# Kernel tuning notes

Measured on AMD Instinct MI355X. Metric: run time of the kernel, lower is better.

The kernel has to match this reference:

```python
import jax, jax.numpy as jnp
import numpy as np

N_NODES = 50000
N_EDGES = 800000
IN_DIM = 128
HID = 128
LATENT = 64
N_LAYERS = 3
N_GRAPHS = 256
BN_EPS = 1e-5


def setup_inputs() -> dict:
    key = jax.random.key(0)
    ks = jax.random.split(key, 12)
    x = jax.random.normal(ks[0], (N_NODES, IN_DIM), dtype=jnp.float32)
    edge_index = jax.random.randint(ks[1], (2, N_EDGES), 0, N_NODES, dtype=jnp.int32)
    batch = jnp.sort(jax.random.randint(ks[2], (N_NODES,), 0, N_GRAPHS, dtype=jnp.int32))
    s = 1.0 / np.sqrt(HID)
    # stacked per-layer SAGEConv params: lin_l (neighbor path, with bias), lin_r (root path)
    Wl = jax.random.uniform(ks[3], (N_LAYERS, HID, HID), jnp.float32, -s, s)
    bl = jax.random.uniform(ks[4], (N_LAYERS, HID), jnp.float32, -s, s)
    Wr = jax.random.uniform(ks[5], (N_LAYERS, HID, HID), jnp.float32, -s, s)
    gamma = jnp.ones((HID,), jnp.float32)
    beta = jnp.zeros((HID,), jnp.float32)
    fcW = jax.random.uniform(ks[6], (HID, LATENT), jnp.float32, -s, s)
    fcb = jax.random.uniform(ks[7], (LATENT,), jnp.float32, -s, s)
    return {"x": x, "edge_index": edge_index, "batch": batch, "Wl": Wl, "bl": bl,
            "Wr": Wr, "gamma": gamma, "beta": beta, "fcW": fcW, "fcb": fcb}


def _sage_conv(x, src, dst, Wl_i, bl_i, Wr_i):
    # mean-aggregate source features into target nodes (PyG SAGEConv, aggr='mean')
    agg = jax.ops.segment_sum(x[src], dst, num_segments=N_NODES)  # [N, D]
    cnt = jax.ops.segment_sum(jnp.ones((src.shape[0],), x.dtype), dst, num_segments=N_NODES)
    mean = agg / jnp.maximum(cnt, 1.0)[:, None]
    return mean @ Wl_i + bl_i + x @ Wr_i


def reference(x, edge_index, batch, Wl, bl, Wr, gamma, beta, fcW, fcb):
    src, dst = edge_index[0], edge_index[1]
    h = x
    for i in range(N_LAYERS):
        h = _sage_conv(h, src, dst, Wl[i], bl[i], Wr[i])
        h = jax.nn.relu(h)  # dropout: identity at inference
    # global_add_pool over graphs
    pooled = jax.ops.segment_sum(h, batch, num_segments=N_GRAPHS)  # [G, HID]
    # BatchNorm1d over the graph dimension (batch statistics)
    mu = pooled.mean(axis=0)
    var = pooled.var(axis=0)
    normed = (pooled - mu) * jax.lax.rsqrt(var + BN_EPS) * gamma + beta
    return normed @ fcW + fcb
```

## Files before the change

kernel.cpp:

```cpp
#include <hip/hip_runtime.h>
#include <cstdint>
#include <cstddef>

constexpr int HID = 128;
constexpr int LATENT = 64;
constexpr int BSHIFT = 7;
constexpr int NBUCK_MAX = 512;
constexpr int EPB = 1024;

typedef __attribute__((ext_vector_type(8))) short short8;
typedef __attribute__((ext_vector_type(4))) float f32x4;

__device__ inline unsigned short f2bf(float f) {
    unsigned u = __float_as_uint(f);
    u += 0x7fff + ((u >> 16) & 1);
    return (unsigned short)(u >> 16);
}
__device__ inline unsigned pack_bf16x2(float lo, float hi) {
    unsigned ulo = __float_as_uint(lo);
    unsigned uhi = __float_as_uint(hi);
    ulo += 0x7fff + ((ulo >> 16) & 1);
    uhi += 0x7fff + ((uhi >> 16) & 1);
    return (ulo >> 16) | (uhi & 0xffff0000u);
}

__global__ __launch_bounds__(256) void stage1_k(const int* __restrict__ dst,
                                                const float* __restrict__ x,
                                                const float* __restrict__ Wl,
                                                const float* __restrict__ Wr,
                                                int* __restrict__ partial,
                                                unsigned* __restrict__ hx2,
                                                unsigned short* __restrict__ WT,
                                                int nE, int nbuck, int ebB, int n2x) {
    if (blockIdx.x < (unsigned)ebB) {
        __shared__ int lh[NBUCK_MAX];
        for (int b = threadIdx.x; b < nbuck; b += 256) lh[b] = 0;
        __syncthreads();
        int base = blockIdx.x * EPB;
        int end = min(base + EPB, nE);
        for (int i = base + threadIdx.x; i < end; i += 256)
            atomicAdd(&lh[dst[i] >> BSHIFT], 1);
        __syncthreads();
        int* row = partial + (size_t)blockIdx.x * NBUCK_MAX;
        for (int b = threadIdx.x; b < nbuck; b += 256) row[b] = lh[b];
    } else if (blockIdx.x < (unsigned)(ebB + 384)) {
        int idx = (blockIdx.x - ebB) * 256 + threadIdx.x;
        int l = idx / (128 * 256);
        int rem = idx % (128 * 256);
        int n = rem / 256;
        int k = rem % 256;
        float v = (k < 128) ? Wl[(size_t)l * 128 * 128 + (size_t)k * 128 + n]
                            : Wr[(size_t)l * 128 * 128 + (size_t)(k - 128) * 128 + n];
        WT[idx] = f2bf(v);
    } else {
        int i = (blockIdx.x - ebB - 384) * 256 + threadIdx.x;
        if (i < n2x) {
            float2 v = ((const float2*)x)[i];
            hx2[i] = pack_bf16x2(v.x, v.y);
        }
    }
}

__global__ __launch_bounds__(256) void colscan_k(int* __restrict__ partial,
                                                 int* __restrict__ bucketTotal, int ebB) {
    int b = blockIdx.x;
    int t = threadIdx.x;
    const int CH = (ebB + 255) / 256;
    int vals[8];
    int s = 0;
    #pragma unroll
    for (int c = 0; c < 8; ++c) {
        if (c >= CH) break;
        int k = t * CH + c;
        int v = (k < ebB) ? partial[(size_t)k * NBUCK_MAX + b] : 0;
        vals[c] = v; s += v;
    }
    __shared__ int part[256];
    part[t] = s;
    __syncthreads();
    for (int d = 1; d < 256; d <<= 1) {
        int u = (t >= d) ? part[t - d] : 0;
        __syncthreads();
        if (t >= d) part[t] += u;
        __syncthreads();
    }
    int run = (t == 0) ? 0 : part[t - 1];
    #pragma unroll
    for (int c = 0; c < 8; ++c) {
        if (c >= CH) break;
        int k = t * CH + c;
        if (k < ebB) partial[(size_t)k * NBUCK_MAX + b] = run;
        run += vals[c];
    }
    if (t == 255) bucketTotal[b] = run;
}

__global__ __launch_bounds__(512) void bscan2_k(const int* __restrict__ bucketTotal,
                                                int* __restrict__ bucketStart,
                                                int* __restrict__ row_ptr,
                                                int nbuck, int nE, int nN) {
    __shared__ int part[512];
    int t = threadIdx.x;
    int v = (t < nbuck) ? bucketTotal[t] : 0;
    part[t] = v;
    __syncthreads();
    for (int d = 1; d < 512; d <<= 1) {
        int u = (t >= d) ? part[t - d] : 0;
        __syncthreads();
        if (t >= d) part[t] += u;
        __syncthreads();
    }
    if (t < nbuck) bucketStart[t] = part[t] - v;
    if (t == 0) { bucketStart[nbuck] = nE; row_ptr[nN] = nE; }
}

__global__ __launch_bounds__(256) void bplace_k(const int* __restrict__ src,
                                                const int* __restrict__ dst,
                                                const int* __restrict__ partial,
                                                const int* __restrict__ bucketStart,
                                                uint2* __restrict__ staged, int nE, int nbuck) {
    __shared__ int lh[NBUCK_MAX];
    __shared__ int lb[NBUCK_MAX];
    for (int b = threadIdx.x; b < nbuck; b += 256) lh[b] = 0;
    __syncthreads();
    int base = blockIdx.x * EPB;
    int end = min(base + EPB, nE);
    const int* myPre = partial + (size_t)blockIdx.x * NBUCK_MAX;
    for (int b = threadIdx.x; b < nbuck; b += 256)
        lb[b] = bucketStart[b] + myPre[b];
    __syncthreads();
    for (int i = base + threadIdx.x; i < end; i += 256) {
        int d = dst[i];
        int b = d >> BSHIFT;
        int loc = atomicAdd(&lh[b], 1);
        staged[lb[b] + loc] = make_uint2((unsigned)src[i], (unsigned)d);
    }
}

__global__ __launch_bounds__(256) void sort_bucket_k(const uint2* __restrict__ staged,
                                                     const int* __restrict__ bucketStart,
                                                     int* __restrict__ row_ptr,
                                                     float* __restrict__ inv,
                                                     int* __restrict__ csr_src, int nN) {
    __shared__ int cnt[128];
    __shared__ int rp[128];
    int g = blockIdx.x;
    int beg = bucketStart[g], end = bucketStart[g + 1];
    if (threadIdx.x < 128) cnt[threadIdx.x] = 0;
    __syncthreads();
    for (int i = beg + threadIdx.x; i < end; i += 256)
        atomicAdd(&cnt[staged[i].y & 127], 1);
    __syncthreads();
    if (threadIdx.x < 128) rp[threadIdx.x] = cnt[threadIdx.x];
    __syncthreads();
    #pragma unroll
    for (int d = 1; d < 128; d <<= 1) {
        int v = 0;
        if (threadIdx.x < 128 && threadIdx.x >= d) v = rp[threadIdx.x - d];
        __syncthreads();
        if (threadIdx.x < 128 && threadIdx.x >= d) rp[threadIdx.x] += v;
        __syncthreads();
    }
    if (threadIdx.x < 128) {
        int c = cnt[threadIdx.x];
        int excl = rp[threadIdx.x] - c;
        int node = (g << BSHIFT) + threadIdx.x;
        if (node < nN) {
            row_ptr[node] = beg + excl;
            inv[node] = 1.0f / fmaxf((float)c, 1.0f);
        }
        cnt[threadIdx.x] = excl;
    }
    __syncthreads();
    for (int i = beg + threadIdx.x; i < end; i += 256) {
        uint2 e = staged[i];
        int pos = atomicAdd(&cnt[e.y & 127], 1);
        csr_src[beg + pos] = (int)e.x;
    }
}

__global__ __launch_bounds__(256) void gather_k(const int* __restrict__ row_ptr,
                                                const int* __restrict__ csr_src,
                                                const float* __restrict__ inv,
                                                const uint4* __restrict__ h4,
                                                uint4* __restrict__ mean4, int nN) {
    int w = blockIdx.x * 4 + (threadIdx.x >> 6);
    if (w >= nN) return;
    int lane = threadIdx.x & 63;
    int quarter = lane >> 4;
    int col = lane & 15;
    int beg = row_ptr[w], end = row_ptr[w + 1];
    float accA[8] = {}, accB[8] = {}, accC[8] = {}, accD[8] = {};
    for (int base = beg; base < end; base += 64) {
        int navail = min(64, end - base);
        int idx = (lane < navail) ? csr_src[base + lane] : 0;
        for (int j = 0; j < navail; j += 16) {
            int e0 = j + quarter;
            int e1 = j + 4 + quarter;
            int e2 = j + 8 + quarter;
            int e3 = j + 12 + quarter;
            int s0 = __shfl(idx, min(e0, navail - 1), 64);
            int s1 = __shfl(idx, min(e1, navail - 1), 64);
            int s2 = __shfl(idx, min(e2, navail - 1), 64);
            int s3 = __shfl(idx, min(e3, navail - 1), 64);
            uint4 u0 = h4[(size_t)s0 * 16 + col];
            uint4 u1 = h4[(size_t)s1 * 16 + col];
            uint4 u2 = h4[(size_t)s2 * 16 + col];
            uint4 u3 = h4[(size_t)s3 * 16 + col];
            if (e0 < navail) {
                accA[0] += __uint_as_float(u0.x << 16); accA[1] += __uint_as_float(u0.x & 0xffff0000u);
                accA[2] += __uint_as_float(u0.y << 16); accA[3] += __uint_as_float(u0.y & 0xffff0000u);
                accA[4] += __uint_as_float(u0.z << 16); accA[5] += __uint_as_float(u0.z & 0xffff0000u);
                accA[6] += __uint_as_float(u0.w << 16); accA[7] += __uint_as_float(u0.w & 0xffff0000u);
            }
            if (e1 < navail) {
                accB[0] += __uint_as_float(u1.x << 16); accB[1] += __uint_as_float(u1.x & 0xffff0000u);
                accB[2] += __uint_as_float(u1.y << 16); accB[3] += __uint_as_float(u1.y & 0xffff0000u);
                accB[4] += __uint_as_float(u1.z << 16); accB[5] += __uint_as_float(u1.z & 0xffff0000u);
                accB[6] += __uint_as_float(u1.w << 16); accB[7] += __uint_as_float(u1.w & 0xffff0000u);
            }
            if (e2 < navail) {
                accC[0] += __uint_as_float(u2.x << 16); accC[1] += __uint_as_float(u2.x & 0xffff0000u);
                accC[2] += __uint_as_float(u2.y << 16); accC[3] += __uint_as_float(u2.y & 0xffff0000u);
                accC[4] += __uint_as_float(u2.z << 16); accC[5] += __uint_as_float(u2.z & 0xffff0000u);
                accC[6] += __uint_as_float(u2.w << 16); accC[7] += __uint_as_float(u2.w & 0xffff0000u);
            }
            if (e3 < navail) {
                accD[0] += __uint_as_float(u3.x << 16); accD[1] += __uint_as_float(u3.x & 0xffff0000u);
                accD[2] += __uint_as_float(u3.y << 16); accD[3] += __uint_as_float(u3.y & 0xffff0000u);
                accD[4] += __uint_as_float(u3.z << 16); accD[5] += __uint_as_float(u3.z & 0xffff0000u);
                accD[6] += __uint_as_float(u3.w << 16); accD[7] += __uint_as_float(u3.w & 0xffff0000u);
            }
        }
    }
    #pragma unroll
    for (int k = 0; k < 8; ++k) {
        float v = (accA[k] + accB[k]) + (accC[k] + accD[k]);
        v += __shfl_xor(v, 16, 64);
        v += __shfl_xor(v, 32, 64);
        accA[k] = v;
    }
    if (quarter == 0) {
        float iv = inv[w];
        uint4 o;
        o.x = pack_bf16x2(accA[0] * iv, accA[1] * iv);
        o.y = pack_bf16x2(accA[2] * iv, accA[3] * iv);
        o.z = pack_bf16x2(accA[4] * iv, accA[5] * iv);
        o.w = pack_bf16x2(accA[6] * iv, accA[7] * iv);
        mean4[(size_t)w * 16 + col] = o;
    }
}

__global__ __launch_bounds__(256) void sage_mfma_k(
    const unsigned short* __restrict__ mean,
    const unsigned short* __restrict__ h,
    const unsigned short* __restrict__ WT,
    const float* __restrict__ bl,
    unsigned short* __restrict__ out, int nN)
{
    __shared__ unsigned short sB[128 * 256];

    {
        int row = threadIdx.x >> 1, half = threadIdx.x & 1;
        const short8* src = (const short8*)(WT + row * 256 + half * 128);
        int sw = (row & 7) << 2;
        #pragma unroll
        for (int j = 0; j < 16; ++j) {
            int unit = half * 16 + j;
            int unit2 = unit ^ sw;
            *(short8*)(sB + row * 256 + unit2 * 8) = src[j];
        }
    }
    __syncthreads();

    const int wave = threadIdx.x >> 6;
    const int lane = threadIdx.x & 63;
    const int m = lane & 15;
    const int q = lane >> 4;
    const int row = blockIdx.x * 64 + wave * 16 + m;
    const int rowc = min(row, nN - 1);
    const int swm = (m & 7) << 2;

    f32x4 acc[8] = {};
    #pragma unroll
    for (int ks = 0; ks < 8; ++ks) {
        const unsigned short* Aptr = (ks < 4) ? mean : h;
        short8 a = *(const short8*)(Aptr + (size_t)rowc * HID + (ks & 3) * 32 + q * 8);
        #pragma unroll
        for (int t = 0; t < 8; ++t) {
            int unit2 = (ks * 4 + q) ^ swm;
            short8 b = *(const short8*)(sB + (t * 16 + m) * 256 + unit2 * 8);
            acc[t] = __builtin_amdgcn_mfma_f32_16x16x32_bf16(a, b, acc[t], 0, 0, 0);
        }
    }

    int orow_base = blockIdx.x * 64 + wave * 16 + q * 4;
    #pragma unroll
    for (int t = 0; t < 8; ++t) {
        float bias = bl[t * 16 + m];
        #pragma unroll
        for (int r = 0; r < 4; ++r) {
            int orow = orow_base + r;
            if (orow < nN) {
                float v = fmaxf(acc[t][r] + bias, 0.f);
                out[(size_t)orow * HID + t * 16 + m] = f2bf(v);
            }
        }
    }
}

__global__ __launch_bounds__(256) void pool_seg_k(const unsigned* __restrict__ h2,
                                                  const int* __restrict__ batch,
                                                  float* __restrict__ pooled, int nN) {
    int g = blockIdx.x;
    int lo = 0, hi = nN;
    while (lo < hi) { int mid = (lo + hi) >> 1; if (batch[mid] < g) lo = mid + 1; else hi = mid; }
    int beg = lo;
    hi = nN;
    while (lo < hi) { int mid = (lo + hi) >> 1; if (batch[mid] <= g) lo = mid + 1; else hi = mid; }
    int end = lo;

    int lane = threadIdx.x & 63;
    int sub  = threadIdx.x >> 6;
    float s0 = 0.f, s1 = 0.f;
    for (int i = beg + sub; i < end; i += 4) {
        unsigned u = h2[(size_t)i * 64 + lane];
        s0 += __uint_as_float(u << 16);
        s1 += __uint_as_float(u & 0xffff0000u);
    }
    __shared__ float red[4][HID];
    red[sub][2 * lane]     = s0;
    red[sub][2 * lane + 1] = s1;
    __syncthreads();
    if (sub == 0) {
        float v0 = red[0][2 * lane] + red[1][2 * lane] + red[2][2 * lane] + red[3][2 * lane];
        float v1 = red[0][2 * lane + 1] + red[1][2 * lane + 1] + red[2][2 * lane + 1] + red[3][2 * lane + 1];
        pooled[(size_t)g * HID + 2 * lane]     = v0;
        pooled[(size_t)g * HID + 2 * lane + 1] = v1;
    }
}

__global__ __launch_bounds__(1024) void bn_stats_k(const float* __restrict__ pooled,
                                                   const float* __restrict__ gamma,
                                                   const float* __restrict__ beta,
                                                   float* __restrict__ scale,
                                                   float* __restrict__ shift, int nG) {
    __shared__ float rs[8][HID], rs2[8][HID];
    int j = threadIdx.x & (HID - 1);
    int stripe = threadIdx.x >> 7;
    float s = 0.f, s2 = 0.f;
    for (int g = stripe; g < nG; g += 8) {
        float v = pooled[(size_t)g * HID + j];
        s += v; s2 += v * v;
    }
    rs[stripe][j] = s; rs2[stripe][j] = s2;
    __syncthreads();
    if (threadIdx.x < HID) {
        float S = 0.f, S2 = 0.f;
        #pragma unroll
        for (int k = 0; k < 8; ++k) { S += rs[k][j]; S2 += rs2[k][j]; }
        float invG = 1.0f / (float)nG;
        float mu = S * invG;
        float var = S2 * invG - mu * mu;
        float r = rsqrtf(var + 1e-5f) * gamma[j];
        scale[j] = r;
        shift[j] = beta[j] - mu * r;
    }
}

__global__ __launch_bounds__(LATENT) void fc_k(const float* __restrict__ pooled,
                                               const float* __restrict__ scale,
                                               const float* __restrict__ shift,
                                               const float* __restrict__ fcW,
                                               const float* __restrict__ fcb,
                                               float* __restrict__ out, int nG) {
    int g = blockIdx.x;
    int o = threadIdx.x;
    float acc = fcb[o];
    for (int j = 0; j < HID; ++j) {
        float v = pooled[(size_t)g * HID + j] * scale[j] + shift[j];
        acc += v * fcW[(size_t)j * LATENT + o];
    }
    out[(size_t)g * LATENT + o] = acc;
}

extern "C" void kernel_launch(void* const* d_in, const int* in_sizes, int n_in,
                              void* d_out, int out_size, void* d_ws, size_t ws_size,
                              hipStream_t stream) {
    const float* x     = (const float*)d_in[0];
    const int*   ei    = (const int*)d_in[1];
    const int*   batch = (const int*)d_in[2];
    const float* Wl    = (const float*)d_in[3];
    const float* bl    = (const float*)d_in[4];
    const float* Wr    = (const float*)d_in[5];
    const float* gamma = (const float*)d_in[6];
    const float* beta  = (const float*)d_in[7];
    const float* fcW   = (const float*)d_in[8];
    const float* fcb   = (const float*)d_in[9];
    float* out = (float*)d_out;

    const int nN = in_sizes[0] / HID;
    const int nE = in_sizes[1] / 2;
    const int nG = out_size / LATENT;
    const int* src = ei;
    const int* dst = ei + nE;
    const int nbuck = (nN + 127) >> BSHIFT;
    const int ebB = (nE + EPB - 1) / EPB;

    unsigned short* hx   = (unsigned short*)d_ws;
    unsigned short* B1   = hx + (size_t)nN * HID;
    unsigned short* B2   = B1 + (size_t)nN * HID;
    unsigned short* mean = B2 + (size_t)nN * HID;
    unsigned short* WT   = mean + (size_t)nN * HID;
    float* inv    = (float*)(WT + 3 * 128 * 256);
    float* pooled = inv + nN;
    float* scale  = pooled + (size_t)nG * HID;
    float* shift  = scale + HID;
    int*   row_ptr     = (int*)(shift + HID);
    int*   csr_src     = row_ptr + (nN + 1);
    int*   bucketStart = csr_src + nE;
    int*   bucketTotal = bucketStart + NBUCK_MAX + 1;
    int*   partial     = bucketTotal + NBUCK_MAX;
    uint2* staged      = (uint2*)mean;

    const int n2x = nN * HID / 2;
    const int convx_blocks = (n2x + 255) / 256;

    stage1_k<<<ebB + 384 + convx_blocks, 256, 0, stream>>>(dst, x, Wl, Wr, partial,
                                                           (unsigned*)hx, WT, nE, nbuck, ebB, n2x);
    colscan_k<<<nbuck, 256, 0, stream>>>(partial, bucketTotal, ebB);
    bscan2_k<<<1, 512, 0, stream>>>(bucketTotal, bucketStart, row_ptr, nbuck, nE, nN);
    bplace_k<<<ebB, 256, 0, stream>>>(src, dst, partial, bucketStart, staged, nE, nbuck);
    sort_bucket_k<<<nbuck, 256, 0, stream>>>(staged, bucketStart, row_ptr, inv, csr_src, nN);

    const int gather_blocks = (nN + 3) / 4;
    const int gemm_blocks = (nN + 63) / 64;

    const unsigned short* hcur = hx;
    unsigned short* outs[3] = {B1, B2, B1};
    for (int l = 0; l < 3; ++l) {
        gather_k<<<gather_blocks, 256, 0, stream>>>(row_ptr, csr_src, inv,
                                                    (const uint4*)hcur, (uint4*)mean, nN);
        sage_mfma_k<<<gemm_blocks, 256, 0, stream>>>(mean, hcur,
                                                     WT + (size_t)l * 128 * 256,
                                                     bl + (size_t)l * HID,
                                                     outs[l], nN);
        hcur = outs[l];
    }

    pool_seg_k<<<nG, 256, 0, stream>>>((const unsigned*)hcur, batch, pooled, nN);
    bn_stats_k<<<1, 1024, 0, stream>>>(pooled, gamma, beta, scale, shift, nG);
    fc_k<<<nG, LATENT, 0, stream>>>(pooled, scale, shift, fcW, fcb, out, nG);
}
```

Measured before the change: 315.5 us.

## Fuse neighbor gather with SAGE MFMA GEMM and fold bucket scan into consumers

Merges the per-layer mean-aggregation kernel and the MFMA GEMM into one 512-thread kernel. Each block aggregates 64 rows into LDS and multiplies them directly, so the bf16 mean buffer no longer makes a round trip through global memory. The GEMM now reads the weight tile straight from global/L2 instead of staging a swizzled copy in LDS. The single-block bucket prefix-scan kernel is removed and its scan is recomputed redundantly inside bplace and sort_bucket blocks, saving a launch at the cost of repeated small scans. Each wave now gathers 8 rows serially, which may reduce latency hiding in the gather phase.

Result: slower. 384.8 us (+22.0%).

```diff
diff --git a/kernel.cpp b/kernel.cpp
--- a/kernel.cpp
+++ b/kernel.cpp
@@ -31,8 +31,10 @@
                                                 int* __restrict__ partial,
                                                 unsigned* __restrict__ hx2,
                                                 unsigned short* __restrict__ WT,
-                                                int nE, int nbuck, int ebB, int n2x) {
+                                                int* __restrict__ row_ptr,
+                                                int nE, int nbuck, int ebB, int n2x, int nN) {
     if (blockIdx.x < (unsigned)ebB) {
+        if (blockIdx.x == 0 && threadIdx.x == 0) row_ptr[nN] = nE;
         __shared__ int lh[NBUCK_MAX];
         for (int b = threadIdx.x; b < nbuck; b += 256) lh[b] = 0;
         __syncthreads();
@@ -95,41 +97,34 @@
     if (t == 255) bucketTotal[b] = run;
 }
 
-__global__ __launch_bounds__(512) void bscan2_k(const int* __restrict__ bucketTotal,
-                                                int* __restrict__ bucketStart,
-                                                int* __restrict__ row_ptr,
-                                                int nbuck, int nE, int nN) {
-    __shared__ int part[512];
-    int t = threadIdx.x;
-    int v = (t < nbuck) ? bucketTotal[t] : 0;
-    part[t] = v;
-    __syncthreads();
-    for (int d = 1; d < 512; d <<= 1) {
-        int u = (t >= d) ? part[t - d] : 0;
-        __syncthreads();
-        if (t >= d) part[t] += u;
-        __syncthreads();
-    }
-    if (t < nbuck) bucketStart[t] = part[t] - v;
-    if (t == 0) { bucketStart[nbuck] = nE; row_ptr[nN] = nE; }
-}
-
 __global__ __launch_bounds__(256) void bplace_k(const int* __restrict__ src,
                                                 const int* __restrict__ dst,
                                                 const int* __restrict__ partial,
-                                                const int* __restrict__ bucketStart,
+                                                const int* __restrict__ bucketTotal,
                                                 uint2* __restrict__ staged, int nE, int nbuck) {
     __shared__ int lh[NBUCK_MAX];
     __shared__ int lb[NBUCK_MAX];
-    for (int b = threadIdx.x; b < nbuck; b += 256) lh[b] = 0;
+    __shared__ int part[256];
+    int t = threadIdx.x;
+    for (int b = t; b < nbuck; b += 256) lh[b] = 0;
+    int v0 = (2 * t < nbuck) ? bucketTotal[2 * t] : 0;
+    int v1 = (2 * t + 1 < nbuck) ? bucketTotal[2 * t + 1] : 0;
+    part[t] = v0 + v1;
+    __syncthreads();
+    for (int d = 1; d < 256; d <<= 1) {
+        int u = (t >= d) ? part[t - d] : 0;
+        __syncthreads();
+        if (t >= d) part[t] += u;
+        __syncthreads();
+    }
+    const int* myPre = partial + (size_t)blockIdx.x * NBUCK_MAX;
+    int excl = part[t] - v0 - v1;
+    if (2 * t < nbuck)     lb[2 * t]     = excl + myPre[2 * t];
+    if (2 * t + 1 < nbuck) lb[2 * t + 1] = excl + v0 + myPre[2 * t + 1];
     __syncthreads();
     int base = blockIdx.x * EPB;
     int end = min(base + EPB, nE);
-    const int* myPre = partial + (size_t)blockIdx.x * NBUCK_MAX;
-    for (int b = threadIdx.x; b < nbuck; b += 256)
-        lb[b] = bucketStart[b] + myPre[b];
-    __syncthreads();
-    for (int i = base + threadIdx.x; i < end; i += 256) {
+    for (int i = base + t; i < end; i += 256) {
         int d = dst[i];
         int b = d >> BSHIFT;
         int loc = atomicAdd(&lh[b], 1);
@@ -138,172 +133,185 @@
 }
 
 __global__ __launch_bounds__(256) void sort_bucket_k(const uint2* __restrict__ staged,
-                                                     const int* __restrict__ bucketStart,
+                                                     const int* __restrict__ bucketTotal,
                                                      int* __restrict__ row_ptr,
                                                      float* __restrict__ inv,
-                                                     int* __restrict__ csr_src, int nN) {
+                                                     int* __restrict__ csr_src, int nN, int nbuck) {
+    __shared__ int part[256];
     __shared__ int cnt[128];
     __shared__ int rp[128];
+    __shared__ int sBeg;
     int g = blockIdx.x;
-    int beg = bucketStart[g], end = bucketStart[g + 1];
-    if (threadIdx.x < 128) cnt[threadIdx.x] = 0;
-    __syncthreads();
-    for (int i = beg + threadIdx.x; i < end; i += 256)
+    int t = threadIdx.x;
+    int v0 = (2 * t < nbuck) ? bucketTotal[2 * t] : 0;
+    int v1 = (2 * t + 1 < nbuck) ? bucketTotal[2 * t + 1] : 0;
+    part[t] = v0 + v1;
+    __syncthreads();
+    for (int d = 1; d < 256; d <<= 1) {
+        int u = (t >= d) ? part[t - d] : 0;
+        __syncthreads();
+        if (t >= d) part[t] += u;
+        __syncthreads();
+    }
+    if (t == (g >> 1)) {
+        int excl = part[t] - v0 - v1;
+        sBeg = (g & 1) ? (excl + v0) : excl;
+    }
+    if (t < 128) cnt[t] = 0;
+    __syncthreads();
+    int beg = sBeg;
+    int end = beg + bucketTotal[g];
+    for (int i = beg + t; i < end; i += 256)
         atomicAdd(&cnt[staged[i].y & 127], 1);
     __syncthreads();
-    if (threadIdx.x < 128) rp[threadIdx.x] = cnt[threadIdx.x];
+    if (t < 128) rp[t] = cnt[t];
     __syncthreads();
     #pragma unroll
     for (int d = 1; d < 128; d <<= 1) {
         int v = 0;
-        if (threadIdx.x < 128 && threadIdx.x >= d) v = rp[threadIdx.x - d];
-        __syncthreads();
-        if (threadIdx.x < 128 && threadIdx.x >= d) rp[threadIdx.x] += v;
-        __syncthreads();
-    }
-    if (threadIdx.x < 128) {
-        int c = cnt[threadIdx.x];
-        int excl = rp[threadIdx.x] - c;
-        int node = (g << BSHIFT) + threadIdx.x;
+        if (t < 128 && t >= d) v = rp[t - d];
+        __syncthreads();
+        if (t < 128 && t >= d) rp[t] += v;
+        __syncthreads();
+    }
+    if (t < 128) {
+        int c = cnt[t];
+        int excl = rp[t] - c;
+        int node = (g << BSHIFT) + t;
         if (node < nN) {
             row_ptr[node] = beg + excl;
             inv[node] = 1.0f / fmaxf((float)c, 1.0f);
         }
-        cnt[threadIdx.x] = excl;
-    }
-    __syncthreads();
-    for (int i = beg + threadIdx.x; i < end; i += 256) {
+        cnt[t] = excl;
+    }
+    __syncthreads();
+    for (int i = beg + t; i < end; i += 256) {
         uint2 e = staged[i];
         int pos = atomicAdd(&cnt[e.y & 127], 1);
         csr_src[beg + pos] = (int)e.x;
     }
 }
 
-__global__ __launch_bounds__(256) void gather_k(const int* __restrict__ row_ptr,
-                                                const int* __restrict__ csr_src,
-                                                const float* __restrict__ inv,
-                                                const uint4* __restrict__ h4,
-                                                uint4* __restrict__ mean4, int nN) {
-    int w = blockIdx.x * 4 + (threadIdx.x >> 6);
-    if (w >= nN) return;
-    int lane = threadIdx.x & 63;
-    int quarter = lane >> 4;
-    int col = lane & 15;
-    int beg = row_ptr[w], end = row_ptr[w + 1];
-    float accA[8] = {}, accB[8] = {}, accC[8] = {}, accD[8] = {};
-    for (int base = beg; base < end; base += 64) {
-        int navail = min(64, end - base);
-        int idx = (lane < navail) ? csr_src[base + lane] : 0;
-        for (int j = 0; j < navail; j += 16) {
-            int e0 = j + quarter;
-            int e1 = j + 4 + quarter;
-            int e2 = j + 8 + quarter;
-            int e3 = j + 12 + quarter;
-            int s0 = __shfl(idx, min(e0, navail - 1), 64);
-            int s1 = __shfl(idx, min(e1, navail - 1), 64);
-            int s2 = __shfl(idx, min(e2, navail - 1), 64);
-            int s3 = __shfl(idx, min(e3, navail - 1), 64);
-            uint4 u0 = h4[(size_t)s0 * 16 + col];
-            uint4 u1 = h4[(size_t)s1 * 16 + col];
-            uint4 u2 = h4[(size_t)s2 * 16 + col];
-            uint4 u3 = h4[(size_t)s3 * 16 + col];
-            if (e0 < navail) {
-                accA[0] += __uint_as_float(u0.x << 16); accA[1] += __uint_as_float(u0.x & 0xffff0000u);
-                accA[2] += __uint_as_float(u0.y << 16); accA[3] += __uint_as_float(u0.y & 0xffff0000u);
-                accA[4] += __uint_as_float(u0.z << 16); accA[5] += __uint_as_float(u0.z & 0xffff0000u);
-                accA[6] += __uint_as_float(u0.w << 16); accA[7] += __uint_as_float(u0.w & 0xffff0000u);
-            }
-            if (e1 < navail) {
-                accB[0] += __uint_as_float(u1.x << 16); accB[1] += __uint_as_float(u1.x & 0xffff0000u);
-                accB[2] += __uint_as_float(u1.y << 16); accB[3] += __uint_as_float(u1.y & 0xffff0000u);
-                accB[4] += __uint_as_float(u1.z << 16); accB[5] += __uint_as_float(u1.z & 0xffff0000u);
-                accB[6] += __uint_as_float(u1.w << 16); accB[7] += __uint_as_float(u1.w & 0xffff0000u);
-            }
-            if (e2 < navail) {
-                accC[0] += __uint_as_float(u2.x << 16); accC[1] += __uint_as_float(u2.x & 0xffff0000u);
-                accC[2] += __uint_as_float(u2.y << 16); accC[3] += __uint_as_float(u2.y & 0xffff0000u);
-                accC[4] += __uint_as_float(u2.z << 16); accC[5] += __uint_as_float(u2.z & 0xffff0000u);
-                accC[6] += __uint_as_float(u2.w << 16); accC[7] += __uint_as_float(u2.w & 0xffff0000u);
-            }
-            if (e3 < navail) {
-                accD[0] += __uint_as_float(u3.x << 16); accD[1] += __uint_as_float(u3.x & 0xffff0000u);
-                accD[2] += __uint_as_float(u3.y << 16); accD[3] += __uint_as_float(u3.y & 0xffff0000u);
-                accD[4] += __uint_as_float(u3.z << 16); accD[5] += __uint_as_float(u3.z & 0xffff0000u);
-                accD[6] += __uint_as_float(u3.w << 16); accD[7] += __uint_as_float(u3.w & 0xffff0000u);
-            }
-        }
-    }
-    #pragma unroll
-    for (int k = 0; k < 8; ++k) {
-        float v = (accA[k] + accB[k]) + (accC[k] + accD[k]);
-        v += __shfl_xor(v, 16, 64);
-        v += __shfl_xor(v, 32, 64);
-        accA[k] = v;
-    }
-    if (quarter == 0) {
-        float iv = inv[w];
-        uint4 o;
-        o.x = pack_bf16x2(accA[0] * iv, accA[1] * iv);
-        o.y = pack_bf16x2(accA[2] * iv, accA[3] * iv);
-        o.z = pack_bf16x2(accA[4] * iv, accA[5] * iv);
-        o.w = pack_bf16x2(accA[6] * iv, accA[7] * iv);
-        mean4[(size_t)w * 16 + col] = o;
-    }
-}
-
-__global__ __launch_bounds__(256) void sage_mfma_k(
-    const unsigned short* __restrict__ mean,
+__global__ __launch_bounds__(512) void layer_fused_k(
+    const int* __restrict__ row_ptr,
+    const int* __restrict__ csr_src,
+    const float* __restrict__ inv,
     const unsigned short* __restrict__ h,
     const unsigned short* __restrict__ WT,
     const float* __restrict__ bl,
     unsigned short* __restrict__ out, int nN)
 {
-    __shared__ unsigned short sB[128 * 256];
-
-    {
-        int row = threadIdx.x >> 1, half = threadIdx.x & 1;
-        const short8* src = (const short8*)(WT + row * 256 + half * 128);
-        int sw = (row & 7) << 2;
-        #pragma unroll
-        for (int j = 0; j < 16; ++j) {
-            int unit = half * 16 + j;
-            int unit2 = unit ^ sw;
-            *(short8*)(sB + row * 256 + unit2 * 8) = src[j];
-        }
-    }
-    __syncthreads();
-
+    __shared__ unsigned short sMean[64][136];
+    const uint4* h4 = (const uint4*)h;
     const int wave = threadIdx.x >> 6;
     const int lane = threadIdx.x & 63;
+    const int quarter = lane >> 4;
+    const int col = lane & 15;
+
+    for (int tn = 0; tn < 8; ++tn) {
+        int r = wave * 8 + tn;
+        int w = blockIdx.x * 64 + r;
+        int wc = min(w, nN - 1);
+        int beg = row_ptr[wc], end = row_ptr[wc + 1];
+        float accA[8] = {}, accB[8] = {}, accC[8] = {}, accD[8] = {};
+        for (int base = beg; base < end; base += 64) {
+            int navail = min(64, end - base);
+            int idx = (lane < navail) ? csr_src[base + lane] : 0;
+            for (int j = 0; j < navail; j += 16) {
+                int e0 = j + quarter;
+                int e1 = j + 4 + quarter;
+                int e2 = j + 8 + quarter;
+                int e3 = j + 12 + quarter;
+                int s0 = __shfl(idx, min(e0, navail - 1), 64);
+                int s1 = __shfl(idx, min(e1, navail - 1), 64);
+                int s2 = __shfl(idx, min(e2, navail - 1), 64);
+                int s3 = __shfl(idx, min(e3, navail - 1), 64);
+                uint4 u0 = h4[(size_t)s0 * 16 + col];
+                uint4 u1 = h4[(size_t)s1 * 16 + col];
+                uint4 u2 = h4[(size_t)s2 * 16 + col];
+                uint4 u3 = h4[(size_t)s3 * 16 + col];
+                if (e0 < navail) {
+                    accA[0] += __uint_as_float(u0.x << 16); accA[1] += __uint_as_float(u0.x & 0xffff0000u);
+                    accA[2] += __uint_as_float(u0.y << 16); accA[3] += __uint_as_float(u0.y & 0xffff0000u);
+                    accA[4] += __uint_as_float(u0.z << 16); accA[5] += __uint_as_float(u0.z & 0xffff0000u);
+                    accA[6] += __uint_as_float(u0.w << 16); accA[7] += __uint_as_float(u0.w & 0xffff0000u);
+                }
+                if (e1 < navail) {
+                    accB[0] += __uint_as_float(u1.x << 16); accB[1] += __uint_as_float(u1.x & 0xffff0000u);
+                    accB[2] += __uint_as_float(u1.y << 16); accB[3] += __uint_as_float(u1.y & 0xffff0000u);
+                    accB[4] += __uint_as_float(u1.z << 16); accB[5] += __uint_as_float(u1.z & 0xffff0000u);
+                    accB[6] += __uint_as_float(u1.w << 16); accB[7] += __uint_as_float(u1.w & 0xffff0000u);
+                }
+                if (e2 < navail) {
+                    accC[0] += __uint_as_float(u2.x << 16); accC[1] += __uint_as_float(u2.x & 0xffff0000u);
+                    accC[2] += __uint_as_float(u2.y << 16); accC[3] += __uint_as_float(u2.y & 0xffff0000u);
+                    accC[4] += __uint_as_float(u2.z << 16); accC[5] += __uint_as_float(u2.z & 0xffff0000u);
+                    accC[6] += __uint_as_float(u2.w << 16); accC[7] += __uint_as_float(u2.w & 0xffff0000u);
+                }
+                if (e3 < navail) {
+                    accD[0] += __uint_as_float(u3.x << 16); accD[1] += __uint_as_float(u3.x & 0xffff0000u);
+                    accD[2] += __uint_as_float(u3.y << 16); accD[3] += __uint_as_float(u3.y & 0xffff0000u);
+                    accD[4] += __uint_as_float(u3.z << 16); accD[5] += __uint_as_float(u3.z & 0xffff0000u);
+                    accD[6] += __uint_as_float(u3.w << 16); accD[7] += __uint_as_float(u3.w & 0xffff0000u);
+                }
+            }
+        }
+        #pragma unroll
+        for (int k = 0; k < 8; ++k) {
+            float v = (accA[k] + accB[k]) + (accC[k] + accD[k]);
+            v += __shfl_xor(v, 16, 64);
+            v += __shfl_xor(v, 32, 64);
+            accA[k] = v;
+        }
+        if (quarter == 0) {
+            float iv = inv[wc];
+            uint4 o;
+            o.x = pack_bf16x2(accA[0] * iv, accA[1] * iv);
+            o.y = pack_bf16x2(accA[2] * iv, accA[3] * iv);
+            o.z = pack_bf16x2(accA[4] * iv, accA[5] * iv);
+            o.w = pack_bf16x2(accA[6] * iv, accA[7] * iv);
+            *(uint4*)&sMean[r][col * 8] = o;
+        }
+    }
+    __syncthreads();
+
     const int m = lane & 15;
-    const int q = lane >> 4;
-    const int row = blockIdx.x * 64 + wave * 16 + m;
-    const int rowc = min(row, nN - 1);
-    const int swm = (m & 7) << 2;
-
-    f32x4 acc[8] = {};
-    #pragma unroll
-    for (int ks = 0; ks < 8; ++ks) {
-        const unsigned short* Aptr = (ks < 4) ? mean : h;
-        short8 a = *(const short8*)(Aptr + (size_t)rowc * HID + (ks & 3) * 32 + q * 8);
+    const int q = quarter;
+    const int rg = wave & 3;
+    const int ch = wave >> 1 >> 1;
+    const int lrow = rg * 16 + m;
+    const int growc = min(blockIdx.x * 64 + lrow, nN - 1);
+
+    short8 a[8];
+    #pragma unroll
+    for (int ks = 0; ks < 4; ++ks)
+        a[ks] = *(const short8*)&sMean[lrow][ks * 32 + q * 8];
+    #pragma unroll
+    for (int ks = 0; ks < 4; ++ks)
+        a[4 + ks] = *(const short8*)(h + (size_t)growc * HID + ks * 32 + q * 8);
+
+    f32x4 acc[4] = {};
+    #pragma unroll
+    for (int tt = 0; tt < 4; ++tt) {
+        int n = (ch * 4 + tt) * 16 + m;
         #pragma unroll
-        for (int t = 0; t < 8; ++t) {
-            int unit2 = (ks * 4 + q) ^ swm;
-            short8 b = *(const short8*)(sB + (t * 16 + m) * 256 + unit2 * 8);
-            acc[t] = __builtin_amdgcn_mfma_f32_16x16x32_bf16(a, b, acc[t], 0, 0, 0);
-        }
-    }
-
-    int orow_base = blockIdx.x * 64 + wave * 16 + q * 4;
-    #pragma unroll
-    for (int t = 0; t < 8; ++t) {
-        float bias = bl[t * 16 + m];
+        for (int ks = 0; ks < 8; ++ks) {
+            short8 b = *(const short8*)(WT + (size_t)n * 256 + (ks * 4 + q) * 8);
+            acc[tt] = __builtin_amdgcn_mfma_f32_16x16x32_bf16(a[ks], b, acc[tt], 0, 0, 0);
+        }
+    }
+
+    int orow_base = blockIdx.x * 64 + rg * 16 + q * 4;
+    #pragma unroll
+    for (int tt = 0; tt < 4; ++tt) {
+        int n = (ch * 4 + tt) * 16 + m;
+        float bias = bl[n];
         #pragma unroll
-        for (int r = 0; r < 4; ++r) {
-            int orow = orow_base + r;
+        for (int r2 = 0; r2 < 4; ++r2) {
+            int orow = orow_base + r2;
             if (orow < nN) {
-                float v = fmaxf(acc[t][r] + bias, 0.f);
-                out[(size_t)orow * HID + t * 16 + m] = f2bf(v);
+                float v = fmaxf(acc[tt][r2] + bias, 0.f);
+                out[(size_t)orow * HID + n] = f2bf(v);
             }
         }
     }
@@ -427,24 +435,21 @@
     const int convx_blocks = (n2x + 255) / 256;
 
     stage1_k<<<ebB + 384 + convx_blocks, 256, 0, stream>>>(dst, x, Wl, Wr, partial,
-                                                           (unsigned*)hx, WT, nE, nbuck, ebB, n2x);
+                                                           (unsigned*)hx, WT, row_ptr,
+                                                           nE, nbuck, ebB, n2x, nN);
     colscan_k<<<nbuck, 256, 0, stream>>>(partial, bucketTotal, ebB);
-    bscan2_k<<<1, 512, 0, stream>>>(bucketTotal, bucketStart, row_ptr, nbuck, nE, nN);
-    bplace_k<<<ebB, 256, 0, stream>>>(src, dst, partial, bucketStart, staged, nE, nbuck);
-    sort_bucket_k<<<nbuck, 256, 0, stream>>>(staged, bucketStart, row_ptr, inv, csr_src, nN);
-
-    const int gather_blocks = (nN + 3) / 4;
-    const int gemm_blocks = (nN + 63) / 64;
+    bplace_k<<<ebB, 256, 0, stream>>>(src, dst, partial, bucketTotal, staged, nE, nbuck);
+    sort_bucket_k<<<nbuck, 256, 0, stream>>>(staged, bucketTotal, row_ptr, inv, csr_src, nN, nbuck);
+
+    const int layer_blocks = (nN + 63) / 64;
 
     const unsigned short* hcur = hx;
     unsigned short* outs[3] = {B1, B2, B1};
     for (int l = 0; l < 3; ++l) {
-        gather_k<<<gather_blocks, 256, 0, stream>>>(row_ptr, csr_src, inv,
-                                                    (const uint4*)hcur, (uint4*)mean, nN);
-        sage_mfma_k<<<gemm_blocks, 256, 0, stream>>>(mean, hcur,
-                                                     WT + (size_t)l * 128 * 256,
-                                                     bl + (size_t)l * HID,
-                                                     outs[l], nN);
+        layer_fused_k<<<layer_blocks, 512, 0, stream>>>(row_ptr, csr_src, inv, hcur,
+                                                        WT + (size_t)l * 128 * 256,
+                                                        bl + (size_t)l * HID,
+                                                        outs[l], nN);
         hcur = outs[l];
     }
 
```
